# Kernel optimization log

Hardware: AMD Instinct MI355X
Metric: run time of the kernel (lower is better)

The kernel has to match this reference:

```python
import jax, jax.numpy as jnp
import numpy as np

ROPE_THETA = 10000.0

def rope(x):
    # RoPE over the FULL model_dim (applied pre head-split, as in the source),
    # interleaved even/odd pairs. x: [B, S, D]
    B, S, D = x.shape
    half = D // 2
    inv_freq = 1.0 / (ROPE_THETA ** (jnp.arange(half, dtype=jnp.float32) * 2.0 / D))
    ang = jnp.arange(S, dtype=jnp.float32)[:, None] * inv_freq[None, :]  # [S, half]
    cos, sin = jnp.cos(ang), jnp.sin(ang)
    x1, x2 = x[..., 0::2], x[..., 1::2]
    r1 = x1 * cos - x2 * sin
    r2 = x1 * sin + x2 * cos
    return jnp.stack([r1, r2], axis=-1).reshape(B, S, D)


def setup_inputs() -> dict:
    key = jax.random.key(0)
    ks = jax.random.split(key, 9)
    B, S, D = 4, 2048, 768
    w = 0.02
    return {
        "X":  jax.random.normal(ks[0], (B, S, D), dtype=jnp.float32),
        "Wq": jax.random.normal(ks[1], (D, D), dtype=jnp.float32) * w,
        "bq": jnp.zeros((D,), dtype=jnp.float32),
        "Wk": jax.random.normal(ks[2], (D, D), dtype=jnp.float32) * w,
        "bk": jnp.zeros((D,), dtype=jnp.float32),
        "Wv": jax.random.normal(ks[3], (D, D), dtype=jnp.float32) * w,
        "bv": jnp.zeros((D,), dtype=jnp.float32),
        "Wo": jax.random.normal(ks[4], (D, D), dtype=jnp.float32) * w,
        "bo": jnp.zeros((D,), dtype=jnp.float32),
    }


def reference(X, Wq, bq, Wk, bk, Wv, bv, Wo, bo):
    NUM_HEADS = 12
    B, S, D = X.shape
    hd = D // NUM_HEADS

    q = rope(X @ Wq + bq)   # RoPE applied pre-split on full model_dim
    k = rope(X @ Wk + bk)
    v = X @ Wv + bv

    # Contiguous per-head slices == reshape to [B, S, H, hd]
    qh = q.reshape(B, S, NUM_HEADS, hd)
    kh = k.reshape(B, S, NUM_HEADS, hd)
    vh = v.reshape(B, S, NUM_HEADS, hd)

    scores = jnp.einsum('bqhd,bkhd->bhqk', qh, kh) / jnp.sqrt(jnp.float32(hd))
    causal = jnp.tril(jnp.ones((S, S), dtype=bool))
    scores = jnp.where(causal[None, None, :, :], scores, -jnp.inf)
    weights = jax.nn.softmax(scores, axis=-1)
    out = jnp.einsum('bhqk,bkhd->bqhd', weights, vh).reshape(B, S, D)
    return out @ Wo + bo
```

## Files before the change

### kernel.cpp

```cpp
#include <hip/hip_runtime.h>
#include <math.h>

#define D_MODEL 768
#define NUM_HEADS 12
#define HEAD_DIM 64
#define SEQ 2048
#define BATCH 4
#define MROWS (BATCH * SEQ)
#define HALF_D (D_MODEL / 2)

typedef __bf16 bf16x8 __attribute__((ext_vector_type(8)));
typedef __bf16 bf16x4 __attribute__((ext_vector_type(4)));
typedef float  f32x4  __attribute__((ext_vector_type(4)));

__device__ __forceinline__ void gload_lds16(const void* gp, void* lp) {
    __builtin_amdgcn_global_load_lds(
        (const __attribute__((address_space(1))) unsigned int*)gp,
        (__attribute__((address_space(3))) unsigned int*)lp, 16, 0, 0);
}

__global__ __launch_bounds__(256)
void prep(const float* __restrict__ X, __bf16* __restrict__ Xb,
          const float* __restrict__ W0, const float* __restrict__ W1,
          const float* __restrict__ W2, const float* __restrict__ W3,
          __bf16* __restrict__ T0, __bf16* __restrict__ T1,
          __bf16* __restrict__ T2, __bf16* __restrict__ T3,
          float2* __restrict__ tab)
{
    __shared__ float t[64][65];
    const int n   = blockIdx.x;
    const int tid = threadIdx.x;

    if (n < 3072) {
        int idx = n * 256 + tid;
        int s = idx / HALF_D;
        int j = idx - s * HALF_D;
        float freq = __expf(-(float)j * (9.210340371976184f / 384.0f));
        float sn, cs;
        sincosf((float)s * freq, &sn, &cs);
        tab[idx] = make_float2(cs, sn);
    } else if (n < 6144) {
        size_t i = ((size_t)(n - 3072) * 256 + tid) * 8;
        float4 u = *(const float4*)(X + i);
        float4 v = *(const float4*)(X + i + 4);
        bf16x8 o;
        o[0]=(__bf16)u.x; o[1]=(__bf16)u.y; o[2]=(__bf16)u.z; o[3]=(__bf16)u.w;
        o[4]=(__bf16)v.x; o[5]=(__bf16)v.y; o[6]=(__bf16)v.z; o[7]=(__bf16)v.w;
        *(bf16x8*)(Xb + i) = o;
    } else {
        int m = n - 6144;
        int z = m / 144;
        int rem = m - z * 144;
        int by = rem / 12, bx = rem % 12;
        const float* W = z == 0 ? W0 : z == 1 ? W1 : z == 2 ? W2 : W3;
        __bf16*      T = z == 0 ? T0 : z == 1 ? T1 : z == 2 ? T2 : T3;

        const int r0 = by * 64, c0 = bx * 64;
        const int lx = tid & 63, g = tid >> 6;

        #pragma unroll
        for (int rr = 0; rr < 16; ++rr) {
            int r = g * 16 + rr;
            t[r][lx] = W[(size_t)(r0 + r) * D_MODEL + c0 + lx];
        }
        __syncthreads();

        const int nn = tid >> 2;
        const int kb = (tid & 3) * 16;
        bf16x8 o1, o2;
        #pragma unroll
        for (int mm = 0; mm < 8; ++mm) o1[mm] = (__bf16)t[kb + mm][nn];
        #pragma unroll
        for (int mm = 0; mm < 8; ++mm) o2[mm] = (__bf16)t[kb + 8 + mm][nn];
        __bf16* dst = T + (size_t)(c0 + nn) * D_MODEL + r0 + kb;
        *(bf16x8*)dst       = o1;
        *(bf16x8*)(dst + 8) = o2;
    }
}

__global__ __launch_bounds__(256)
void qkv_gemm(const __bf16* __restrict__ Xb,
              const __bf16* __restrict__ Wqt, const __bf16* __restrict__ Wkt,
              const __bf16* __restrict__ Wvt,
              const float* __restrict__ bq, const float* __restrict__ bk,
              const float* __restrict__ bv,
              const float2* __restrict__ tab,
              __bf16* __restrict__ Qb, __bf16* __restrict__ Kb,
              __bf16* __restrict__ Vtb)
{
    __shared__ bf16x8 Asf[2][8][64];
    __shared__ bf16x8 Bsf[2][8][64];

    const int tid  = threadIdx.x;
    const int wv   = tid >> 6;
    const int ln   = tid & 63;
    const int t15  = ln & 15;
    const int quad = ln >> 4;
    const int wr = wv >> 1, wc = wv & 1;

    const int lin = blockIdx.x;
    const int c   = lin >> 6;
    const int r   = lin & 63;
    const int which = c / 6;
    const int col0  = (c % 6) * 128;
    const int row0  = r * 128;

    const __bf16* Wt  = which == 0 ? Wqt : which == 1 ? Wkt : Wvt;
    const float* bias = which == 0 ? bq  : which == 1 ? bk  : bv;

    f32x4 acc[4][4];
    #pragma unroll
    for (int i = 0; i < 4; ++i)
        #pragma unroll
        for (int j = 0; j < 4; ++j) acc[i][j] = (f32x4){0.f,0.f,0.f,0.f};

    const __bf16* a0 = Xb + (size_t)(row0 + 16 * wv       + t15) * D_MODEL + 8 * quad;
    const __bf16* a1 = Xb + (size_t)(row0 + 16 * (wv + 4) + t15) * D_MODEL + 8 * quad;
    const __bf16* b0 = Wt + (size_t)(col0 + 16 * wv       + t15) * D_MODEL + 8 * quad;
    const __bf16* b1 = Wt + (size_t)(col0 + 16 * (wv + 4) + t15) * D_MODEL + 8 * quad;

    for (int k0 = 0; k0 < D_MODEL; k0 += 64) {
        __syncthreads();
        #pragma unroll
        for (int ks = 0; ks < 2; ++ks) {
            const int kk = k0 + 32 * ks;
            gload_lds16(a0 + kk, &Asf[ks][wv][0]);
            gload_lds16(a1 + kk, &Asf[ks][wv + 4][0]);
            gload_lds16(b0 + kk, &Bsf[ks][wv][0]);
            gload_lds16(b1 + kk, &Bsf[ks][wv + 4][0]);
        }
        __syncthreads();

        #pragma unroll
        for (int ks = 0; ks < 2; ++ks) {
            bf16x8 af[4], bfr[4];
            #pragma unroll
            for (int i = 0; i < 4; ++i) af[i]  = Asf[ks][4 * wr + i][ln];
            #pragma unroll
            for (int j = 0; j < 4; ++j) bfr[j] = Bsf[ks][4 * wc + j][ln];
            #pragma unroll
            for (int i = 0; i < 4; ++i)
                #pragma unroll
                for (int j = 0; j < 4; ++j)
                    acc[i][j] = __builtin_amdgcn_mfma_f32_16x16x32_bf16(af[i], bfr[j], acc[i][j], 0, 0, 0);
        }
    }

    #pragma unroll
    for (int i = 0; i < 4; ++i) {
        const int rowb = row0 + 64 * wr + 16 * i + 4 * quad;
        #pragma unroll
        for (int j = 0; j < 4; ++j) {
            const int col = col0 + 64 * wc + 16 * j + t15;
            const float bval = bias[col];
            if (which < 2) {
                const int jh  = col >> 1;
                const float sgn = (col & 1) ? 1.0f : -1.0f;
                const float oscale = (which == 0) ? 0.125f : 1.0f;
                __bf16* dst = (which ? Kb : Qb);
                #pragma unroll
                for (int rr = 0; rr < 4; ++rr) {
                    const int rw = rowb + rr;
                    const int s  = rw & (SEQ - 1);
                    float val  = acc[i][j][rr] + bval;
                    float part = __shfl_xor(val, 1, 64);
                    float2 cs  = tab[(size_t)s * HALF_D + jh];
                    dst[(size_t)rw * D_MODEL + col] = (__bf16)((val * cs.x + part * sgn * cs.y) * oscale);
                }
            } else {
                const int h = col >> 6, d = col & 63;
                const int bidx = rowb >> 11, s = rowb & (SEQ - 1);
                bf16x4 pk;
                #pragma unroll
                for (int rr = 0; rr < 4; ++rr) pk[rr] = (__bf16)(acc[i][j][rr] + bval);
                *(bf16x4*)(Vtb + ((size_t)(bidx * NUM_HEADS + h) * 64 + d) * SEQ + s) = pk;
            }
        }
    }
}

__global__ __launch_bounds__(256)
void out_gemm(const __bf16* __restrict__ Ab, const __bf16* __restrict__ Wt,
              const float* __restrict__ bias, float* __restrict__ Cout)
{
    __shared__ bf16x8 Asf[2][8][64];
    __shared__ bf16x8 Bsf[2][8][64];

    const int tid  = threadIdx.x;
    const int wv   = tid >> 6;
    const int ln   = tid & 63;
    const int t15  = ln & 15;
    const int quad = ln >> 4;
    const int wr = wv >> 1, wc = wv & 1;

    const int lin = blockIdx.x;
    const int col0 = (lin >> 6) * 128;
    const int row0 = (lin & 63) * 128;

    f32x4 acc[4][4];
    #pragma unroll
    for (int i = 0; i < 4; ++i)
        #pragma unroll
        for (int j = 0; j < 4; ++j) acc[i][j] = (f32x4){0.f,0.f,0.f,0.f};

    const __bf16* a0 = Ab + (size_t)(row0 + 16 * wv       + t15) * D_MODEL + 8 * quad;
    const __bf16* a1 = Ab + (size_t)(row0 + 16 * (wv + 4) + t15) * D_MODEL + 8 * quad;
    const __bf16* b0 = Wt + (size_t)(col0 + 16 * wv       + t15) * D_MODEL + 8 * quad;
    const __bf16* b1 = Wt + (size_t)(col0 + 16 * (wv + 4) + t15) * D_MODEL + 8 * quad;

    for (int k0 = 0; k0 < D_MODEL; k0 += 64) {
        __syncthreads();
        #pragma unroll
        for (int ks = 0; ks < 2; ++ks) {
            const int kk = k0 + 32 * ks;
            gload_lds16(a0 + kk, &Asf[ks][wv][0]);
            gload_lds16(a1 + kk, &Asf[ks][wv + 4][0]);
            gload_lds16(b0 + kk, &Bsf[ks][wv][0]);
            gload_lds16(b1 + kk, &Bsf[ks][wv + 4][0]);
        }
        __syncthreads();

        #pragma unroll
        for (int ks = 0; ks < 2; ++ks) {
            bf16x8 af[4], bfr[4];
            #pragma unroll
            for (int i = 0; i < 4; ++i) af[i]  = Asf[ks][4 * wr + i][ln];
            #pragma unroll
            for (int j = 0; j < 4; ++j) bfr[j] = Bsf[ks][4 * wc + j][ln];
            #pragma unroll
            for (int i = 0; i < 4; ++i)
                #pragma unroll
                for (int j = 0; j < 4; ++j)
                    acc[i][j] = __builtin_amdgcn_mfma_f32_16x16x32_bf16(af[i], bfr[j], acc[i][j], 0, 0, 0);
        }
    }

    #pragma unroll
    for (int i = 0; i < 4; ++i) {
        const int rowb = row0 + 64 * wr + 16 * i + 4 * quad;
        #pragma unroll
        for (int j = 0; j < 4; ++j) {
            const int col = col0 + 64 * wc + 16 * j + t15;
            const float bval = bias[col];
            #pragma unroll
            for (int rr = 0; rr < 4; ++rr)
                Cout[(size_t)(rowb + rr) * D_MODEL + col] = acc[i][j][rr] + bval;
        }
    }
}

__device__ __forceinline__ void attn_tile(
    const bf16x8 (*Kbuf)[64], const bf16x8 (*Vbuf)[64],
    __bf16 (*Psw)[72],
    bf16x8 aq0, bf16x8 aq1,
    f32x4* o, float* lacc,
    int ln, int t15, int quad, int j0, int qabs, bool domask)
{
    f32x4 s[4];
    #pragma unroll
    for (int c = 0; c < 4; ++c) {
        s[c] = (f32x4){0.f, 0.f, 0.f, 0.f};
        s[c] = __builtin_amdgcn_mfma_f32_16x16x32_bf16(aq0, Kbuf[c][ln],     s[c], 0, 0, 0);
        s[c] = __builtin_amdgcn_mfma_f32_16x16x32_bf16(aq1, Kbuf[4 + c][ln], s[c], 0, 0, 0);
    }

    float p[4][4];
    #pragma unroll
    for (int c = 0; c < 4; ++c)
        #pragma unroll
        for (int r = 0; r < 4; ++r) {
            float e = __expf(s[c][r]);
            if (domask && (j0 + 16 * c + t15 > qabs + r)) e = 0.f;
            p[c][r] = e;
            lacc[r] += e;
        }

    #pragma unroll
    for (int c = 0; c < 4; ++c)
        #pragma unroll
        for (int r = 0; r < 4; ++r)
            Psw[4 * quad + r][16 * c + t15] = (__bf16)p[c][r];
    __asm__ volatile("s_waitcnt lgkmcnt(0)" ::: "memory");

    bf16x8 ap0 = *(const bf16x8*)&Psw[t15][8 * quad];
    bf16x8 ap1 = *(const bf16x8*)&Psw[t15][32 + 8 * quad];

    #pragma unroll
    for (int c = 0; c < 4; ++c) {
        o[c] = __builtin_amdgcn_mfma_f32_16x16x32_bf16(ap0, Vbuf[c][ln],     o[c], 0, 0, 0);
        o[c] = __builtin_amdgcn_mfma_f32_16x16x32_bf16(ap1, Vbuf[4 + c][ln], o[c], 0, 0, 0);
    }
}

__global__ __launch_bounds__(512)
void attn_flash(const __bf16* __restrict__ Q, const __bf16* __restrict__ K,
                const __bf16* __restrict__ Vt, __bf16* __restrict__ O)
{
    __shared__ bf16x8 Kf[2][8][64];
    __shared__ bf16x8 Vf[2][8][64];
    __shared__ __bf16 Psb[8][16][72];

    const int tid  = threadIdx.x;
    const int wv   = tid >> 6;
    const int ln   = tid & 63;
    const int t15  = ln & 15;
    const int quad = ln >> 4;

    const int n  = blockIdx.x;
    const int qt = 15 - (n / 48);
    const int bh = n % 48;
    const int b  = bh / NUM_HEADS;
    const int h  = bh % NUM_HEADS;
    const int q0 = qt * 128;
    const int nt = (q0 >> 6) + 2;

    bf16x8 aq0, aq1;
    {
        const __bf16* qs = Q + (size_t)(b * SEQ + q0 + 16 * wv + t15) * D_MODEL + h * 64 + 8 * quad;
        aq0 = *(const bf16x8*)qs;
        aq1 = *(const bf16x8*)(qs + 32);
    }

    const __bf16* kp = K  + ((size_t)b * SEQ + 16 * (wv & 3) + t15) * D_MODEL
                          + h * 64 + 32 * (wv >> 2) + 8 * quad;
    const __bf16* vp = Vt + ((size_t)bh * 64 + 16 * (wv & 3) + t15) * SEQ
                          + 32 * (wv >> 2) + 8 * quad;

    f32x4 o[4];
    #pragma unroll
    for (int c = 0; c < 4; ++c) o[c] = (f32x4){0.f,0.f,0.f,0.f};
    float lacc[4] = {0.f, 0.f, 0.f, 0.f};
    const int qabs = q0 + 16 * wv + 4 * quad;
    const int wmax = q0 + 16 * wv + 15;

    gload_lds16(kp, &Kf[0][wv][0]);
    gload_lds16(vp, &Vf[0][wv][0]);

    int cur = 0;
    for (int it = 0; it < nt; ++it) {
        __syncthreads();
        if (it + 1 < nt) {
            const int jn = (it + 1) * 64;
            gload_lds16(kp + (size_t)jn * D_MODEL, &Kf[cur ^ 1][wv][0]);
            gload_lds16(vp + jn,                   &Vf[cur ^ 1][wv][0]);
        }
        const int j0 = it * 64;
        if (j0 <= wmax) {
            const bool domask = (j0 + 63) > (q0 + 16 * wv);
            attn_tile(Kf[cur], Vf[cur], Psb[wv], aq0, aq1, o, lacc,
                      ln, t15, quad, j0, qabs, domask);
        }
        cur ^= 1;
    }

    #pragma unroll
    for (int off = 1; off < 16; off <<= 1)
        #pragma unroll
        for (int r = 0; r < 4; ++r)
            lacc[r] += __shfl_xor(lacc[r], off, 64);

    float inv[4];
    #pragma unroll
    for (int r = 0; r < 4; ++r) inv[r] = 1.0f / lacc[r];
    #pragma unroll
    for (int c = 0; c < 4; ++c)
        #pragma unroll
        for (int r = 0; r < 4; ++r) {
            int row = qabs + r;
            O[(size_t)(b * SEQ + row) * D_MODEL + h * 64 + 16 * c + t15] = (__bf16)(o[c][r] * inv[r]);
        }
}

extern "C" void kernel_launch(void* const* d_in, const int* in_sizes, int n_in,
                              void* d_out, int out_size, void* d_ws, size_t ws_size,
                              hipStream_t stream) {
    const float* X  = (const float*)d_in[0];
    const float* Wq = (const float*)d_in[1];
    const float* bq = (const float*)d_in[2];
    const float* Wk = (const float*)d_in[3];
    const float* bk = (const float*)d_in[4];
    const float* Wv = (const float*)d_in[5];
    const float* bv = (const float*)d_in[6];
    const float* Wo = (const float*)d_in[7];
    const float* bo = (const float*)d_in[8];
    float* out = (float*)d_out;

    const size_t BSD = (size_t)MROWS * D_MODEL;
    const size_t WSZ = (size_t)D_MODEL * D_MODEL;

    __bf16* Xb  = (__bf16*)d_ws;
    __bf16* Qb  = Xb  + BSD;
    __bf16* Kb  = Qb  + BSD;
    __bf16* Vtb = Kb  + BSD;
    __bf16* Ob  = Vtb + BSD;
    __bf16* Wqt = Ob  + BSD;
    __bf16* Wkt = Wqt + WSZ;
    __bf16* Wvt = Wkt + WSZ;
    __bf16* Wot = Wvt + WSZ;
    float2* Tab = (float2*)(Wot + WSZ);

    prep<<<6720, 256, 0, stream>>>(X, Xb, Wq, Wk, Wv, Wo, Wqt, Wkt, Wvt, Wot, Tab);

    qkv_gemm<<<1152, 256, 0, stream>>>(Xb, Wqt, Wkt, Wvt, bq, bk, bv, Tab, Qb, Kb, Vtb);

    attn_flash<<<768, 512, 0, stream>>>(Qb, Kb, Vtb, Ob);

    out_gemm<<<384, 256, 0, stream>>>(Ob, Wot, bo, out);
}
```

Measured before the change: 264.0 us.

## Compute RoPE angles inline and halve out_gemm row tile

Drops the precomputed cos/sin table from the prep kernel and computes RoPE frequencies and fast sin/cos directly in the QKV GEMM epilogue. This removes the table-build blocks and the per-element table reads. The output projection GEMM switches to 64x128 tiles with a redistributed load mapping, doubling the block count to fill more CUs. The trade-offs are lower-precision fast trig at large angles and less operand reuse per block in out_gemm.

```diff
diff --git a/kernel.cpp b/kernel.cpp
--- a/kernel.cpp
+++ b/kernel.cpp
@@ -24,23 +24,14 @@
           const float* __restrict__ W0, const float* __restrict__ W1,
           const float* __restrict__ W2, const float* __restrict__ W3,
           __bf16* __restrict__ T0, __bf16* __restrict__ T1,
-          __bf16* __restrict__ T2, __bf16* __restrict__ T3,
-          float2* __restrict__ tab)
+          __bf16* __restrict__ T2, __bf16* __restrict__ T3)
 {
     __shared__ float t[64][65];
     const int n   = blockIdx.x;
     const int tid = threadIdx.x;
 
     if (n < 3072) {
-        int idx = n * 256 + tid;
-        int s = idx / HALF_D;
-        int j = idx - s * HALF_D;
-        float freq = __expf(-(float)j * (9.210340371976184f / 384.0f));
-        float sn, cs;
-        sincosf((float)s * freq, &sn, &cs);
-        tab[idx] = make_float2(cs, sn);
-    } else if (n < 6144) {
-        size_t i = ((size_t)(n - 3072) * 256 + tid) * 8;
+        size_t i = ((size_t)n * 256 + tid) * 8;
         float4 u = *(const float4*)(X + i);
         float4 v = *(const float4*)(X + i + 4);
         bf16x8 o;
@@ -48,7 +39,7 @@
         o[4]=(__bf16)v.x; o[5]=(__bf16)v.y; o[6]=(__bf16)v.z; o[7]=(__bf16)v.w;
         *(bf16x8*)(Xb + i) = o;
     } else {
-        int m = n - 6144;
+        int m = n - 3072;
         int z = m / 144;
         int rem = m - z * 144;
         int by = rem / 12, bx = rem % 12;
@@ -84,7 +75,6 @@
               const __bf16* __restrict__ Wvt,
               const float* __restrict__ bq, const float* __restrict__ bk,
               const float* __restrict__ bv,
-              const float2* __restrict__ tab,
               __bf16* __restrict__ Qb, __bf16* __restrict__ Kb,
               __bf16* __restrict__ Vtb)
 {
@@ -154,7 +144,8 @@
             const int col = col0 + 64 * wc + 16 * j + t15;
             const float bval = bias[col];
             if (which < 2) {
-                const int jh  = col >> 1;
+                const int ne = col & ~1;
+                const float fr = __expf((float)ne * (-9.210340371976184f / 768.0f));
                 const float sgn = (col & 1) ? 1.0f : -1.0f;
                 const float oscale = (which == 0) ? 0.125f : 1.0f;
                 __bf16* dst = (which ? Kb : Qb);
@@ -164,8 +155,10 @@
                     const int s  = rw & (SEQ - 1);
                     float val  = acc[i][j][rr] + bval;
                     float part = __shfl_xor(val, 1, 64);
-                    float2 cs  = tab[(size_t)s * HALF_D + jh];
-                    dst[(size_t)rw * D_MODEL + col] = (__bf16)((val * cs.x + part * sgn * cs.y) * oscale);
+                    float ang  = (float)s * fr;
+                    float cs   = __cosf(ang);
+                    float sn   = __sinf(ang);
+                    dst[(size_t)rw * D_MODEL + col] = (__bf16)((val * cs + part * sgn * sn) * oscale);
                 }
             } else {
                 const int h = col >> 6, d = col & 63;
@@ -183,7 +176,7 @@
 void out_gemm(const __bf16* __restrict__ Ab, const __bf16* __restrict__ Wt,
               const float* __restrict__ bias, float* __restrict__ Cout)
 {
-    __shared__ bf16x8 Asf[2][8][64];
+    __shared__ bf16x8 Asf[2][4][64];
     __shared__ bf16x8 Bsf[2][8][64];
 
     const int tid  = threadIdx.x;
@@ -193,42 +186,44 @@
     const int quad = ln >> 4;
     const int wr = wv >> 1, wc = wv & 1;
 
-    const int lin = blockIdx.x;
-    const int col0 = (lin >> 6) * 128;
-    const int row0 = (lin & 63) * 128;
-
-    f32x4 acc[4][4];
-    #pragma unroll
-    for (int i = 0; i < 4; ++i)
+    const int lin  = blockIdx.x;
+    const int col0 = (lin >> 7) * 128;
+    const int row0 = (lin & 127) * 64;
+
+    f32x4 acc[2][4];
+    #pragma unroll
+    for (int i = 0; i < 2; ++i)
         #pragma unroll
         for (int j = 0; j < 4; ++j) acc[i][j] = (f32x4){0.f,0.f,0.f,0.f};
 
-    const __bf16* a0 = Ab + (size_t)(row0 + 16 * wv       + t15) * D_MODEL + 8 * quad;
-    const __bf16* a1 = Ab + (size_t)(row0 + 16 * (wv + 4) + t15) * D_MODEL + 8 * quad;
-    const __bf16* b0 = Wt + (size_t)(col0 + 16 * wv       + t15) * D_MODEL + 8 * quad;
-    const __bf16* b1 = Wt + (size_t)(col0 + 16 * (wv + 4) + t15) * D_MODEL + 8 * quad;
-
     for (int k0 = 0; k0 < D_MODEL; k0 += 64) {
         __syncthreads();
         #pragma unroll
+        for (int u = 0; u < 6; ++u) {
+            const int id = wv * 6 + u;
+            const int ks = id / 12;
+            const int w  = id % 12;
+            if (w < 4) {
+                const __bf16* src = Ab + (size_t)(row0 + 16 * w + t15) * D_MODEL
+                                       + k0 + 32 * ks + 8 * quad;
+                gload_lds16(src, &Asf[ks][w][0]);
+            } else {
+                const __bf16* src = Wt + (size_t)(col0 + 16 * (w - 4) + t15) * D_MODEL
+                                       + k0 + 32 * ks + 8 * quad;
+                gload_lds16(src, &Bsf[ks][w - 4][0]);
+            }
+        }
+        __syncthreads();
+
+        #pragma unroll
         for (int ks = 0; ks < 2; ++ks) {
-            const int kk = k0 + 32 * ks;
-            gload_lds16(a0 + kk, &Asf[ks][wv][0]);
-            gload_lds16(a1 + kk, &Asf[ks][wv + 4][0]);
-            gload_lds16(b0 + kk, &Bsf[ks][wv][0]);
-            gload_lds16(b1 + kk, &Bsf[ks][wv + 4][0]);
-        }
-        __syncthreads();
-
-        #pragma unroll
-        for (int ks = 0; ks < 2; ++ks) {
-            bf16x8 af[4], bfr[4];
-            #pragma unroll
-            for (int i = 0; i < 4; ++i) af[i]  = Asf[ks][4 * wr + i][ln];
+            bf16x8 af[2], bfr[4];
+            #pragma unroll
+            for (int i = 0; i < 2; ++i) af[i]  = Asf[ks][2 * wr + i][ln];
             #pragma unroll
             for (int j = 0; j < 4; ++j) bfr[j] = Bsf[ks][4 * wc + j][ln];
             #pragma unroll
-            for (int i = 0; i < 4; ++i)
+            for (int i = 0; i < 2; ++i)
                 #pragma unroll
                 for (int j = 0; j < 4; ++j)
                     acc[i][j] = __builtin_amdgcn_mfma_f32_16x16x32_bf16(af[i], bfr[j], acc[i][j], 0, 0, 0);
@@ -236,8 +231,8 @@
     }
 
     #pragma unroll
-    for (int i = 0; i < 4; ++i) {
-        const int rowb = row0 + 64 * wr + 16 * i + 4 * quad;
+    for (int i = 0; i < 2; ++i) {
+        const int rowb = row0 + 32 * wr + 16 * i + 4 * quad;
         #pragma unroll
         for (int j = 0; j < 4; ++j) {
             const int col = col0 + 64 * wc + 16 * j + t15;
@@ -397,13 +392,12 @@
     __bf16* Wkt = Wqt + WSZ;
     __bf16* Wvt = Wkt + WSZ;
     __bf16* Wot = Wvt + WSZ;
-    float2* Tab = (float2*)(Wot + WSZ);
-
-    prep<<<6720, 256, 0, stream>>>(X, Xb, Wq, Wk, Wv, Wo, Wqt, Wkt, Wvt, Wot, Tab);
-
-    qkv_gemm<<<1152, 256, 0, stream>>>(Xb, Wqt, Wkt, Wvt, bq, bk, bv, Tab, Qb, Kb, Vtb);
+
+    prep<<<3648, 256, 0, stream>>>(X, Xb, Wq, Wk, Wv, Wo, Wqt, Wkt, Wvt, Wot);
+
+    qkv_gemm<<<1152, 256, 0, stream>>>(Xb, Wqt, Wkt, Wvt, bq, bk, bv, Qb, Kb, Vtb);
 
     attn_flash<<<768, 512, 0, stream>>>(Qb, Kb, Vtb, Ob);
 
-    out_gemm<<<384, 256, 0, stream>>>(Ob, Wot, bo, out);
-}
+    out_gemm<<<768, 256, 0, stream>>>(Ob, Wot, bo, out);
+}
```

New measurement: 250.7 us. -5.1%, faster.
